# Optimization experiments

Measured on AMD Instinct MI355X. Metric: run time of the kernel, lower is better.

Reference implementation:

```python
import jax, jax.numpy as jnp
import numpy as np


def setup_inputs() -> dict:
    key = jax.random.key(0)
    k1, k2, k3 = jax.random.split(key, 3)
    B, N, D = 16, 512, 256
    # integer frame durations per token, 4..11 frames (avg ~7.5)
    durations = jax.random.randint(k1, (B, N), 4, 12, dtype=jnp.int32)
    # T = max over batch of total frames (static python int, mirrors torch.arange(0, max(s)))
    total_len = int(jnp.max(jnp.sum(durations, axis=-1)))
    x = jax.random.normal(k2, (B, N, D), dtype=jnp.float32)
    # positive Gaussian range (std) per token
    ranges = jax.random.uniform(k3, (B, N), minval=0.5, maxval=4.0, dtype=jnp.float32)
    return {"x": x, "durations": durations, "ranges": ranges, "total_len": total_len}


def _gaussian_weights(durations, ranges, total_len):
    # e: cumulative end frame per token, c: Gaussian center per token
    e = jnp.cumsum(durations, axis=-1).astype(jnp.float32)          # [B, N]
    c = (e - 0.5 * durations.astype(jnp.float32))[..., None]        # [B, N, 1]
    t = jnp.arange(total_len, dtype=jnp.float32)[None, None, :]     # [1, 1, T]
    inv_r2 = ranges[..., None] ** (-2)                               # [B, N, 1]
    w1 = jnp.exp(-inv_r2 * (t - c) ** 2)                             # [B, N, T]
    # original computes the exp twice (w_1 and inside w_2); same math, computed once
    w2 = jnp.sum(w1, axis=1, keepdims=True) + 1e-20                  # [B, 1, T]
    return w1 / w2


def _create_positions(durations, total_len):
    # frame-index-within-token positions: pos[b, t] = t - start_of_segment(t)
    e = jnp.cumsum(durations, axis=-1)                               # [B, N]
    starts = e - durations                                           # [B, N]
    t = jnp.arange(total_len, dtype=durations.dtype)                 # [T]
    seg = jax.vmap(lambda eb: jnp.searchsorted(eb, t, side='right'))(e)  # [B, T]
    seg = jnp.clip(seg, 0, durations.shape[-1] - 1)
    return t[None, :] - jnp.take_along_axis(starts, seg, axis=-1)    # [B, T]


def reference(x, durations, ranges, total_len):
    weights = _gaussian_weights(durations, ranges, total_len)        # [B, N, T]
    # matmul(weights.transpose(1,2), x) -> [B, T, D]
    out = jnp.einsum('bnt,bnd->btd', weights, x)
    positions = _create_positions(durations, total_len)
    return positions, out, weights
```

## Files before the change

kernel.cpp:

```cpp
#include <hip/hip_runtime.h>
#include <hip/hip_bf16.h>


#define TT  64
#define NWC 44
#define KP  64
#define WSS 45
#define WBS 72
#define MARGIN 42.0f

typedef __attribute__((ext_vector_type(8))) short short8;
typedef __attribute__((ext_vector_type(8))) unsigned short ushort8;
typedef __attribute__((ext_vector_type(4))) float f32x4;

__device__ inline unsigned short f2bf(float f) {
    union { float f; unsigned int u; } v; v.f = f;
    unsigned int u = v.u;
    return (unsigned short)((u + 0x7FFFu + ((u >> 16) & 1u)) >> 16);
}

__global__ void scan_kernel(const int* __restrict__ dur,
                            const float* __restrict__ ranges,
                            float* __restrict__ c, float* __restrict__ ir,
                            int* __restrict__ e_i, int* __restrict__ st_i) {
    const int N = 512;
    int b = blockIdx.x, tid = threadIdx.x;
    __shared__ int sc[512];
    int d = dur[b * N + tid];
    sc[tid] = d;
    __syncthreads();
    for (int off = 1; off < 512; off <<= 1) {
        int add = (tid >= off) ? sc[tid - off] : 0;
        __syncthreads();
        sc[tid] += add;
        __syncthreads();
    }
    int e = sc[tid];
    float r = ranges[b * N + tid];
    c[b * N + tid]    = (float)e - 0.5f * (float)d;
    ir[b * N + tid]   = 1.0f / (r * r);
    e_i[b * N + tid]  = e;
    st_i[b * N + tid] = e - d;
}

__global__ __launch_bounds__(256) void wout_kernel(
        const float* __restrict__ x, const float* __restrict__ c,
        const float* __restrict__ ir,
        const int* __restrict__ e_i, const int* __restrict__ st_i,
        float* __restrict__ pos_out ,
        float* __restrict__ out1 , float* __restrict__ out2 ,
        int T) {
    const int N = 512, D = 256;
    int b = blockIdx.y;
    int t0 = blockIdx.x * TT;
    int tid = threadIdx.x;

    __shared__ float c_s[512];
    __shared__ float ir_s[512];
    __shared__ int   es[512], ss[512];
    __shared__ float w_s[TT][WSS];
    __shared__ __align__(16) unsigned short wb[TT][WBS];
    __shared__ float part[4][TT];
    __shared__ float iw2_s[TT];
    __shared__ int lohi[2];

    for (int i = tid; i < 512; i += 256) {
        c_s[i]  = c[b * N + i];
        ir_s[i] = ir[b * N + i];
        es[i]   = e_i[b * N + i];
        ss[i]   = st_i[b * N + i];
    }
    __syncthreads();

    if (tid == 0) {
        float lo_v = (float)t0 - MARGIN;
        float hi_v = (float)(t0 + TT - 1) + MARGIN;
        int lo = 0, hi = 512;
        while (lo < hi) { int m = (lo + hi) >> 1; if (c_s[m] < lo_v) lo = m + 1; else hi = m; }
        int l = lo;
        lo = 0; hi = 512;
        while (lo < hi) { int m = (lo + hi) >> 1; if (c_s[m] <= hi_v) lo = m + 1; else hi = m; }
        int h = lo - 1;
        if (h > l + NWC - 1) h = l + NWC - 1;
        lohi[0] = l; lohi[1] = h;
    }
    if (tid < TT) {
        int t = t0 + tid;
        if (t < T) {
            int lo = 0, hi = 512;
            while (lo < hi) { int m = (lo + hi) >> 1; if (es[m] <= t) lo = m + 1; else hi = m; }
            int seg = min(lo, 511);
            pos_out[b * T + t] = (float)(t - ss[seg]);
        }
    }
    __syncthreads();
    int lo_u = lohi[0], hi_u = lohi[1];

    int tl = tid & 63;
    int s  = tid >> 6;
    int t  = t0 + tl;

    float p = 0.f;
    #pragma unroll
    for (int jj = 0; jj < 16; jj++) {
        int i = s + 4 * jj;
        int n = lo_u + i;
        float w1 = 0.f;
        if (n <= hi_u && t < T) {
            float d = (float)t - c_s[n];
            w1 = __expf(-ir_s[n] * d * d) == 0.f ? 0.f : expf(-ir_s[n] * d * d);
        }
        wb[tl][i] = f2bf(w1);
        if (i < NWC) w_s[tl][i] = w1;
        p += w1;
    }
    part[s][tl] = p;
    __syncthreads();
    if (tid < TT) {
        float w2 = part[0][tid] + part[1][tid] + part[2][tid] + part[3][tid];
        iw2_s[tid] = 1.0f / (w2 + 1e-20f);
    }
    __syncthreads();

    int lane = tid & 63;
    int l15  = lane & 15;
    int q    = lane >> 4;

    f32x4 acc[16];
    #pragma unroll
    for (int nt = 0; nt < 16; nt++) acc[nt] = (f32x4){0.f, 0.f, 0.f, 0.f};

    const float* xb = x + (size_t)b * N * D;
    #pragma unroll
    for (int ks = 0; ks < 2; ks++) {
        short8 afrag = *(const short8*)&wb[16 * s + l15][ks * 32 + q * 8];
        const float* rp[8];
        #pragma unroll
        for (int j = 0; j < 8; j++) {
            int tok = lo_u + ks * 32 + q * 8 + j;
            tok = min(tok, 511);
            rp[j] = xb + (size_t)tok * D;
        }
        #pragma unroll
        for (int nt = 0; nt < 16; nt++) {
            int d = nt * 16 + l15;
            ushort8 bu;
            #pragma unroll
            for (int j = 0; j < 8; j++) bu[j] = f2bf(rp[j][d]);
            short8 bfrag = (short8)bu;
            acc[nt] = __builtin_amdgcn_mfma_f32_16x16x32_bf16(afrag, bfrag, acc[nt], 0, 0, 0);
        }
    }

    float iwq[4];
    #pragma unroll
    for (int r = 0; r < 4; r++) iwq[r] = iw2_s[16 * s + q * 4 + r];
    #pragma unroll
    for (int r = 0; r < 4; r++) {
        int tt = t0 + 16 * s + q * 4 + r;
        if (tt < T) {
            float* orow = out1 + ((size_t)b * T + tt) * D;
            #pragma unroll
            for (int nt = 0; nt < 16; nt++)
                orow[nt * 16 + l15] = acc[nt][r] * iwq[r];
        }
    }

    if (t < T) {
        size_t wbase = (size_t)b * N * T + t;
        float iw2 = iw2_s[tl];
        for (int j = 0; j < 512; j += 4) {
            int nn = j + s;
            int i = nn - lo_u;
            float v = 0.f;
            if (i >= 0 && nn <= hi_u) v = w_s[tl][i] * iw2;
            out2[wbase + (size_t)nn * T] = v;
        }
    }
}

extern "C" void kernel_launch(void* const* d_in, const int* in_sizes, int n_in,
                              void* d_out, int out_size, void* d_ws, size_t ws_size,
                              hipStream_t stream) {
    const float* x      = (const float*)d_in[0];
    const int*   dur    = (const int*)d_in[1];
    const float* ranges = (const float*)d_in[2];
    const int B = 16, N = 512, D = 256;
    const int T = out_size / (B * (1 + D + N));

    float* pos_out = (float*)d_out;
    float* out1    = pos_out + (size_t)B * T;
    float* out2    = out1 + (size_t)B * T * D;

    float* c    = (float*)d_ws;
    float* ir   = c + B * N;
    int*   e_i  = (int*)(ir + B * N);
    int*   st_i = e_i + B * N;

    scan_kernel<<<B, 512, 0, stream>>>(dur, ranges, c, ir, e_i, st_i);

    dim3 g3((T + TT - 1) / TT, B);
    wout_kernel<<<g3, 256, 0, stream>>>(x, c, ir, e_i, st_i, pos_out, out1, out2, T);
}
```

Baseline: 233.9 us.

## Split weights output into separate row-major kernel with vectorized stores

```diff
diff --git a/kernel.cpp b/kernel.cpp
--- a/kernel.cpp
+++ b/kernel.cpp
@@ -4,10 +4,9 @@
 
 #define TT  64
 #define NWC 44
-#define KP  64
-#define WSS 45
 #define WBS 72
 #define MARGIN 42.0f
+#define RPB 8
 
 typedef __attribute__((ext_vector_type(8))) short short8;
 typedef __attribute__((ext_vector_type(8))) unsigned short ushort8;
@@ -43,12 +42,13 @@
     st_i[b * N + tid] = e - d;
 }
 
-__global__ __launch_bounds__(256) void wout_kernel(
+__global__ __launch_bounds__(256) void pass1_kernel(
         const float* __restrict__ x, const float* __restrict__ c,
         const float* __restrict__ ir,
         const int* __restrict__ e_i, const int* __restrict__ st_i,
         float* __restrict__ pos_out ,
-        float* __restrict__ out1 , float* __restrict__ out2 ,
+        float* __restrict__ out1 ,
+        float* __restrict__ iw2_ws ,
         int T) {
     const int N = 512, D = 256;
     int b = blockIdx.y;
@@ -58,7 +58,6 @@
     __shared__ float c_s[512];
     __shared__ float ir_s[512];
     __shared__ int   es[512], ss[512];
-    __shared__ float w_s[TT][WSS];
     __shared__ __align__(16) unsigned short wb[TT][WBS];
     __shared__ float part[4][TT];
     __shared__ float iw2_s[TT];
@@ -108,17 +107,19 @@
         float w1 = 0.f;
         if (n <= hi_u && t < T) {
             float d = (float)t - c_s[n];
-            w1 = __expf(-ir_s[n] * d * d) == 0.f ? 0.f : expf(-ir_s[n] * d * d);
+            w1 = expf(-ir_s[n] * d * d);
         }
         wb[tl][i] = f2bf(w1);
-        if (i < NWC) w_s[tl][i] = w1;
         p += w1;
     }
     part[s][tl] = p;
     __syncthreads();
     if (tid < TT) {
         float w2 = part[0][tid] + part[1][tid] + part[2][tid] + part[3][tid];
-        iw2_s[tid] = 1.0f / (w2 + 1e-20f);
+        float iw2 = 1.0f / (w2 + 1e-20f);
+        iw2_s[tid] = iw2;
+        int t2 = t0 + tid;
+        if (t2 < T) iw2_ws[b * T + t2] = iw2;
     }
     __syncthreads();
 
@@ -152,29 +153,74 @@
         }
     }
 
-    float iwq[4];
-    #pragma unroll
-    for (int r = 0; r < 4; r++) iwq[r] = iw2_s[16 * s + q * 4 + r];
     #pragma unroll
     for (int r = 0; r < 4; r++) {
         int tt = t0 + 16 * s + q * 4 + r;
         if (tt < T) {
+            float iw2 = iw2_s[16 * s + q * 4 + r];
             float* orow = out1 + ((size_t)b * T + tt) * D;
             #pragma unroll
             for (int nt = 0; nt < 16; nt++)
-                orow[nt * 16 + l15] = acc[nt][r] * iwq[r];
-        }
-    }
-
-    if (t < T) {
-        size_t wbase = (size_t)b * N * T + t;
-        float iw2 = iw2_s[tl];
-        for (int j = 0; j < 512; j += 4) {
-            int nn = j + s;
-            int i = nn - lo_u;
-            float v = 0.f;
-            if (i >= 0 && nn <= hi_u) v = w_s[tl][i] * iw2;
-            out2[wbase + (size_t)nn * T] = v;
+                orow[nt * 16 + l15] = acc[nt][r] * iw2;
+        }
+    }
+}
+
+__global__ __launch_bounds__(256) void weights_kernel(
+        const float* __restrict__ c, const float* __restrict__ ir,
+        const float* __restrict__ iw2_ws,
+        float* __restrict__ out2 , int T) {
+    const int N = 512;
+    int b = blockIdx.y;
+    int n0 = blockIdx.x * RPB;
+    int tid = threadIdx.x;
+
+    for (int r = 0; r < RPB; r++) {
+        int n = n0 + r;
+        float cn  = c[b * N + n];
+        float irn = ir[b * N + n];
+        float rad = 10.3f * __frsqrt_rn(irn) + 1.0f;
+        int lo = (int)(cn - rad); if (lo < 0) lo = 0;
+        int hi = (int)(cn + rad) + 1; if (hi > T) hi = T;
+
+        size_t base = ((size_t)b * N + n) * (size_t)T;
+        int head = (int)((4 - (base & 3)) & 3);
+        if (head > T) head = T;
+        if (tid < head) {
+            int t = tid;
+            float w = 0.f;
+            if (t >= lo && t < hi) {
+                float d = (float)t - cn;
+                w = expf(-irn * d * d) * iw2_ws[b * T + t];
+            }
+            out2[base + t] = w;
+        }
+        int ngrp = (T - head) >> 2;
+        int tail = (T - head) & 3;
+        float* rowp = (float*)(out2 + base + head);
+        for (int g = tid; g < ngrp; g += 256) {
+            int tg = head + 4 * g;
+            f32x4 v = (f32x4){0.f, 0.f, 0.f, 0.f};
+            if (tg + 3 >= lo && tg < hi) {
+                #pragma unroll
+                for (int k = 0; k < 4; k++) {
+                    int t = tg + k;
+                    if (t >= lo && t < hi) {
+                        float d = (float)t - cn;
+                        v[k] = expf(-irn * d * d) * iw2_ws[b * T + t];
+                    }
+                }
+            }
+            *(f32x4*)(rowp + 4 * g) = v;
+        }
+        if (tid < tail) {
+            int t = head + 4 * ngrp + tid;
+            float w = 0.f;
+            if (t >= lo && t < hi) {
+                float d = (float)t - cn;
+                w = expf(-irn * d * d) * iw2_ws[b * T + t];
+            }
+            out2[base + t] = w;
         }
     }
 }
@@ -192,13 +238,17 @@
     float* out1    = pos_out + (size_t)B * T;
     float* out2    = out1 + (size_t)B * T * D;
 
-    float* c    = (float*)d_ws;
-    float* ir   = c + B * N;
-    int*   e_i  = (int*)(ir + B * N);
-    int*   st_i = e_i + B * N;
+    float* c      = (float*)d_ws;
+    float* ir     = c + B * N;
+    int*   e_i    = (int*)(ir + B * N);
+    int*   st_i   = e_i + B * N;
+    float* iw2_ws = (float*)(st_i + B * N);
 
     scan_kernel<<<B, 512, 0, stream>>>(dur, ranges, c, ir, e_i, st_i);
 
-    dim3 g3((T + TT - 1) / TT, B);
-    wout_kernel<<<g3, 256, 0, stream>>>(x, c, ir, e_i, st_i, pos_out, out1, out2, T);
-}
+    dim3 g1((T + TT - 1) / TT, B);
+    pass1_kernel<<<g1, 256, 0, stream>>>(x, c, ir, e_i, st_i, pos_out, out1, iw2_ws, T);
+
+    dim3 g2(N / RPB, B);
+    weights_kernel<<<g2, 256, 0, stream>>>(c, ir, iw2_ws, out2, T);
+}
```

Result: faster. 223.6 us (-4.4%).
